# Kernel optimization log

Hardware: AMD Instinct MI355X
Metric: run time of the kernel (lower is better)

The kernel has to match this reference:

```python
import jax, jax.numpy as jnp
import numpy as np

GH, GW, GC = 256, 256, 8  # learned warp grid shape
TWO_PI = 2.0 * np.pi


def setup_inputs() -> dict:
    key = jax.random.key(0)
    k1, k2 = jax.random.split(key)
    image = jax.random.normal(k1, (16, 512, 512, 4), dtype=jnp.float32)
    weight = jax.random.normal(k2, (GH, GW, GC), dtype=jnp.float32)
    return {"image": image, "weight": weight}


def reference(image, weight):
    # typ != 'xyz': map interleaved (x, y) channel pairs to angular coords in [0, 1)
    # image[..., 0::2] -> x coords, image[..., 1::2] -> y coords; each [B,H,W,2]
    C = np.pi - jnp.arctan2(image[..., 1::2], -image[..., 0::2])
    C = C / TWO_PI
    shape_mult = jnp.asarray([GH, GW], dtype=jnp.float32)  # broadcasts over [B,H,W,2]
    C = C * (shape_mult - 1.0)
    C = jnp.clip(C, 0.0, shape_mult - 2.0)

    # bilinear interpolation into weight grid [GH, GW, GC]
    w = C - jnp.floor(C)                      # fractional parts [B,H,W,2]
    w0, w1 = w[..., 0:1], w[..., 1:2]         # [B,H,W,1] each
    idx = C.astype(jnp.int32)
    i0, j0 = idx[..., 0], idx[..., 1]          # [B,H,W]

    def corner(di, dj):
        return weight[i0 + di, j0 + dj]        # gather -> [B,H,W,GC]

    res = (corner(0, 0) * (1.0 - w0) * (1.0 - w1)
           + corner(1, 0) * w0 * (1.0 - w1)
           + corner(0, 1) * (1.0 - w0) * w1
           + corner(1, 1) * w0 * w1)

    W = res * 0.0005                           # [B,H,W,GC]
    return jnp.concatenate([W, image], axis=3)  # [B,H,W,GC+4]
```

## Files before the change

kernel.cpp:

```cpp
#include <hip/hip_runtime.h>
#include <math.h>


#define GH 256
#define GW 256
#define GC 8

__device__ __forceinline__ float4 f4_mad(float4 a, float s, float4 acc) {
    acc.x = fmaf(a.x, s, acc.x);
    acc.y = fmaf(a.y, s, acc.y);
    acc.z = fmaf(a.z, s, acc.z);
    acc.w = fmaf(a.w, s, acc.w);
    return acc;
}

__global__ __launch_bounds__(256) void warp_kernel(
    const float4* __restrict__ img,
    const float*  __restrict__ weight,
    float4*       __restrict__ out,
    int npix)
{
    int p = blockIdx.x * blockDim.x + threadIdx.x;
    if (p >= npix) return;

    float4 px = img[p];

    const float PI = 3.14159265358979323846f;
    const float SCALE = 255.0f / (2.0f * PI);

    float c0 = (PI - atan2f(px.y, -px.x)) * SCALE;
    float c1 = (PI - atan2f(px.w, -px.z)) * SCALE;

    c0 = fminf(fmaxf(c0, 0.0f), 254.0f);
    c1 = fminf(fmaxf(c1, 0.0f), 254.0f);

    int i0 = (int)c0;
    int j0 = (int)c1;
    float w0 = c0 - (float)i0;
    float w1 = c1 - (float)j0;

    float f00 = (1.0f - w0) * (1.0f - w1);
    float f10 = w0 * (1.0f - w1);
    float f01 = (1.0f - w0) * w1;
    float f11 = w0 * w1;

    const float4* wq = (const float4*)weight;
    int b00 = (i0 * GW + j0) * 2;
    int b10 = b00 + GW * 2;

    float4 q00a = wq[b00],     q00b = wq[b00 + 1];
    float4 q01a = wq[b00 + 2], q01b = wq[b00 + 3];
    float4 q10a = wq[b10],     q10b = wq[b10 + 1];
    float4 q11a = wq[b10 + 2], q11b = wq[b10 + 3];

    float4 ra = make_float4(0.f, 0.f, 0.f, 0.f);
    ra = f4_mad(q00a, f00, ra);
    ra = f4_mad(q10a, f10, ra);
    ra = f4_mad(q01a, f01, ra);
    ra = f4_mad(q11a, f11, ra);

    float4 rb = make_float4(0.f, 0.f, 0.f, 0.f);
    rb = f4_mad(q00b, f00, rb);
    rb = f4_mad(q10b, f10, rb);
    rb = f4_mad(q01b, f01, rb);
    rb = f4_mad(q11b, f11, rb);

    const float OUT_SCALE = 0.0005f;
    ra.x *= OUT_SCALE; ra.y *= OUT_SCALE; ra.z *= OUT_SCALE; ra.w *= OUT_SCALE;
    rb.x *= OUT_SCALE; rb.y *= OUT_SCALE; rb.z *= OUT_SCALE; rb.w *= OUT_SCALE;

    int ob = p * 3;
    out[ob]     = ra;
    out[ob + 1] = rb;
    out[ob + 2] = px;
}

extern "C" void kernel_launch(void* const* d_in, const int* in_sizes, int n_in,
                              void* d_out, int out_size, void* d_ws, size_t ws_size,
                              hipStream_t stream) {
    const float4* img    = (const float4*)d_in[0];
    const float*  weight = (const float*)d_in[1];
    float4*       out    = (float4*)d_out;

    int npix = in_sizes[0] / 4;
    int block = 256;
    int grid = (npix + block - 1) / block;

    warp_kernel<<<grid, block, 0, stream>>>(img, weight, out, npix);
}
```

Baseline: 338.3 us.

## Stage weight gathers and output stores through LDS for coalesced access

Threads first publish their corner base addresses to shared memory, then cooperatively gather the 8 float4 weight vectors per pixel, with each group of 8 consecutive threads covering one pixel. The results go into a swizzled LDS buffer. The 48-byte-per-pixel output is also staged through LDS so that the global stores become fully contiguous per block. This targets the strided stores and scattered gathers, at the cost of four barriers and 32KB of LDS per block, which may reduce occupancy.

```diff
diff --git a/kernel.cpp b/kernel.cpp
--- a/kernel.cpp
+++ b/kernel.cpp
@@ -4,7 +4,6 @@
 
 #define GH 256
 #define GW 256
-#define GC 8
 
 __device__ __forceinline__ float4 f4_mad(float4 a, float s, float4 acc) {
     acc.x = fmaf(a.x, s, acc.x);
@@ -16,75 +15,109 @@
 
 __global__ __launch_bounds__(256) void warp_kernel(
     const float4* __restrict__ img,
-    const float*  __restrict__ weight,
+    const float4* __restrict__ wq,
     float4*       __restrict__ out,
     int npix)
 {
-    int p = blockIdx.x * blockDim.x + threadIdx.x;
-    if (p >= npix) return;
+    __shared__ float4 lds_g[2048];
+    __shared__ int    lds_a[256];
 
+    const int t    = threadIdx.x;
+    const int base = blockIdx.x * 256;
+
+    const float PI    = 3.14159265358979323846f;
+    const float SCALE = 255.0f / (2.0f * PI);
+    const float OUT_SCALE = 0.0005f;
+
+    if (base + 256 > npix) {
+        int p = base + t;
+        if (p >= npix) return;
+        float4 px = img[p];
+        float c0 = (PI - atan2f(px.y, -px.x)) * SCALE;
+        float c1 = (PI - atan2f(px.w, -px.z)) * SCALE;
+        c0 = fminf(fmaxf(c0, 0.0f), 254.0f);
+        c1 = fminf(fmaxf(c1, 0.0f), 254.0f);
+        int i0 = (int)c0, j0 = (int)c1;
+        float w0 = c0 - (float)i0, w1 = c1 - (float)j0;
+        float f00 = (1.0f - w0) * (1.0f - w1), f10 = w0 * (1.0f - w1);
+        float f01 = (1.0f - w0) * w1,          f11 = w0 * w1;
+        int b00 = (i0 * GW + j0) * 2, b10 = b00 + GW * 2;
+        float4 ra = make_float4(0,0,0,0), rb = make_float4(0,0,0,0);
+        ra = f4_mad(wq[b00],   f00, ra); rb = f4_mad(wq[b00+1], f00, rb);
+        ra = f4_mad(wq[b00+2], f01, ra); rb = f4_mad(wq[b00+3], f01, rb);
+        ra = f4_mad(wq[b10],   f10, ra); rb = f4_mad(wq[b10+1], f10, rb);
+        ra = f4_mad(wq[b10+2], f11, ra); rb = f4_mad(wq[b10+3], f11, rb);
+        ra.x*=OUT_SCALE; ra.y*=OUT_SCALE; ra.z*=OUT_SCALE; ra.w*=OUT_SCALE;
+        rb.x*=OUT_SCALE; rb.y*=OUT_SCALE; rb.z*=OUT_SCALE; rb.w*=OUT_SCALE;
+        int ob = p * 3;
+        out[ob] = ra; out[ob+1] = rb; out[ob+2] = px;
+        return;
+    }
+
+    int p = base + t;
     float4 px = img[p];
-
-    const float PI = 3.14159265358979323846f;
-    const float SCALE = 255.0f / (2.0f * PI);
-
     float c0 = (PI - atan2f(px.y, -px.x)) * SCALE;
     float c1 = (PI - atan2f(px.w, -px.z)) * SCALE;
-
     c0 = fminf(fmaxf(c0, 0.0f), 254.0f);
     c1 = fminf(fmaxf(c1, 0.0f), 254.0f);
+    int i0 = (int)c0, j0 = (int)c1;
+    float w0 = c0 - (float)i0, w1 = c1 - (float)j0;
+    lds_a[t] = (i0 * GW + j0) * 2;
+    __syncthreads();
 
-    int i0 = (int)c0;
-    int j0 = (int)c1;
-    float w0 = c0 - (float)i0;
-    float w1 = c1 - (float)j0;
+    #pragma unroll
+    for (int k = 0; k < 8; k++) {
+        int g  = t + (k << 8);
+        int pp = g >> 3;
+        int hc = g & 7;
+        int h  = hc >> 2;
+        int c  = hc & 3;
+        int addr = lds_a[pp] + h * (GW * 2) + c;
+        float4 v = wq[addr];
+        lds_g[pp * 8 + (hc ^ (pp & 7))] = v;
+    }
+    __syncthreads();
+
+    float4 q[8];
+    #pragma unroll
+    for (int c2 = 0; c2 < 8; c2++)
+        q[c2] = lds_g[t * 8 + (c2 ^ (t & 7))];
 
     float f00 = (1.0f - w0) * (1.0f - w1);
     float f10 = w0 * (1.0f - w1);
     float f01 = (1.0f - w0) * w1;
     float f11 = w0 * w1;
 
-    const float4* wq = (const float4*)weight;
-    int b00 = (i0 * GW + j0) * 2;
-    int b10 = b00 + GW * 2;
+    float4 ra = make_float4(0,0,0,0), rb = make_float4(0,0,0,0);
+    ra = f4_mad(q[0], f00, ra); rb = f4_mad(q[1], f00, rb);
+    ra = f4_mad(q[2], f01, ra); rb = f4_mad(q[3], f01, rb);
+    ra = f4_mad(q[4], f10, ra); rb = f4_mad(q[5], f10, rb);
+    ra = f4_mad(q[6], f11, ra); rb = f4_mad(q[7], f11, rb);
+    ra.x*=OUT_SCALE; ra.y*=OUT_SCALE; ra.z*=OUT_SCALE; ra.w*=OUT_SCALE;
+    rb.x*=OUT_SCALE; rb.y*=OUT_SCALE; rb.z*=OUT_SCALE; rb.w*=OUT_SCALE;
 
-    float4 q00a = wq[b00],     q00b = wq[b00 + 1];
-    float4 q01a = wq[b00 + 2], q01b = wq[b00 + 3];
-    float4 q10a = wq[b10],     q10b = wq[b10 + 1];
-    float4 q11a = wq[b10 + 2], q11b = wq[b10 + 3];
+    __syncthreads();
+    lds_g[t * 3 + 0] = ra;
+    lds_g[t * 3 + 1] = rb;
+    lds_g[t * 3 + 2] = px;
+    __syncthreads();
 
-    float4 ra = make_float4(0.f, 0.f, 0.f, 0.f);
-    ra = f4_mad(q00a, f00, ra);
-    ra = f4_mad(q10a, f10, ra);
-    ra = f4_mad(q01a, f01, ra);
-    ra = f4_mad(q11a, f11, ra);
-
-    float4 rb = make_float4(0.f, 0.f, 0.f, 0.f);
-    rb = f4_mad(q00b, f00, rb);
-    rb = f4_mad(q10b, f10, rb);
-    rb = f4_mad(q01b, f01, rb);
-    rb = f4_mad(q11b, f11, rb);
-
-    const float OUT_SCALE = 0.0005f;
-    ra.x *= OUT_SCALE; ra.y *= OUT_SCALE; ra.z *= OUT_SCALE; ra.w *= OUT_SCALE;
-    rb.x *= OUT_SCALE; rb.y *= OUT_SCALE; rb.z *= OUT_SCALE; rb.w *= OUT_SCALE;
-
-    int ob = p * 3;
-    out[ob]     = ra;
-    out[ob + 1] = rb;
-    out[ob + 2] = px;
+    int ob = base * 3;
+    out[ob + t]       = lds_g[t];
+    out[ob + 256 + t] = lds_g[256 + t];
+    out[ob + 512 + t] = lds_g[512 + t];
 }
 
 extern "C" void kernel_launch(void* const* d_in, const int* in_sizes, int n_in,
                               void* d_out, int out_size, void* d_ws, size_t ws_size,
                               hipStream_t stream) {
-    const float4* img    = (const float4*)d_in[0];
-    const float*  weight = (const float*)d_in[1];
-    float4*       out    = (float4*)d_out;
+    const float4* img = (const float4*)d_in[0];
+    const float4* wq  = (const float4*)d_in[1];
+    float4*       out = (float4*)d_out;
 
     int npix = in_sizes[0] / 4;
     int block = 256;
     int grid = (npix + block - 1) / block;
 
-    warp_kernel<<<grid, block, 0, stream>>>(img, weight, out, npix);
+    warp_kernel<<<grid, block, 0, stream>>>(img, wq, out, npix);
 }
```

Measured after the change: 282.4 us. 16.5% less time.
